# Kernel optimization log

Measured on AMD Instinct MI355X. Metric: run time of the kernel, lower is better.

Reference implementation:

```python
import jax, jax.numpy as jnp
import numpy as np

EPS = 1e-6

def _rms_norm(x, w):
    rms = jnp.sqrt(jnp.mean(x * x, axis=-1, keepdims=True) + EPS)
    return x / rms * w

def _rotate_half(x):
    x1, x2 = jnp.split(x, 2, axis=-1)
    return jnp.concatenate([-x2, x1], axis=-1)

def _apply_rope(qk, cos, sin):
    return qk * cos + _rotate_half(qk) * sin

def setup_inputs() -> dict:
    key = jax.random.key(0)
    ks = jax.random.split(key, 4)
    B, N, C, H = 4, 2048, 1024, 16
    hd = C // H
    x = jax.random.normal(ks[0], (B, N, C), dtype=jnp.float32)
    rope_cos = jax.random.uniform(ks[1], (1, 1, N, hd), dtype=jnp.float32)
    rope_sin = jax.random.uniform(ks[2], (1, 1, N, hd), dtype=jnp.float32)
    w_qkv = jax.random.normal(ks[3], (3 * C, C), dtype=jnp.float32) * (C ** -0.5)
    w_proj = jax.random.normal(jax.random.fold_in(key, 10), (C, C), dtype=jnp.float32) * (C ** -0.5)
    b_proj = jnp.zeros((C,), dtype=jnp.float32)
    q_norm_w = jnp.ones((hd,), dtype=jnp.float32)
    k_norm_w = jnp.ones((hd,), dtype=jnp.float32)
    return {"x": x, "rope_cos": rope_cos, "rope_sin": rope_sin, "w_qkv": w_qkv,
            "w_proj": w_proj, "b_proj": b_proj, "q_norm_w": q_norm_w, "k_norm_w": k_norm_w}

def reference(x, rope_cos, rope_sin, w_qkv, w_proj, b_proj, q_norm_w, k_norm_w):
    B, N, C = x.shape
    H = 16
    hd = C // H
    scale = hd ** -0.5
    qkv = jnp.einsum('bnc,dc->bnd', x, w_qkv)          # [B,N,3C]
    qkv = qkv.reshape(B, N, 3, H, hd).transpose(2, 0, 3, 1, 4)  # [3,B,H,N,hd]
    q, k, v = qkv[0], qkv[1], qkv[2]
    q = _rms_norm(q, q_norm_w)
    k = _rms_norm(k, k_norm_w)
    q = _apply_rope(q, rope_cos, rope_sin)
    k = _apply_rope(k, rope_cos, rope_sin)
    attn = jnp.einsum('bhqd,bhkd->bhqk', q, k) * scale
    attn = jax.nn.softmax(attn, axis=-1)
    out = jnp.einsum('bhqk,bhkd->bhqd', attn, v)        # [B,H,N,hd]
    out = out.transpose(0, 2, 1, 3).reshape(B, N, C)
    return jnp.einsum('bnc,dc->bnd', out, w_proj) + b_proj
```

## Files before the change

### kernel.cpp

```cpp
#include <hip/hip_runtime.h>
#include <stdint.h>
#include <math.h>

typedef unsigned short u16;
typedef __attribute__((ext_vector_type(8))) short short8;
typedef __attribute__((ext_vector_type(4))) float floatx4;
typedef __attribute__((ext_vector_type(4))) unsigned short ushort4v;

#define MFMA16(a, b, c) __builtin_amdgcn_mfma_f32_16x16x32_bf16(a, b, c, 0, 0, 0)

constexpr int B_ = 4, N_ = 2048, C_ = 1024, H_ = 16, HD = 64;
constexpr size_t SZ_X = (size_t)B_ * N_ * C_;
constexpr size_t SZ_WQKV = (size_t)3 * C_ * C_;
constexpr size_t SZ_WPROJ = (size_t)C_ * C_;
constexpr size_t SZ_QKV = (size_t)B_ * H_ * N_ * HD;

#define QSCALE 0.1803368801111204f

__device__ __forceinline__ u16 f2bf(float f) {
  union { float f; uint32_t u; } c; c.f = f;
  uint32_t u = c.u;
  return (u16)((u + 0x7FFFu + ((u >> 16) & 1u)) >> 16);
}
__device__ __forceinline__ uint32_t p2b(float s) {
  return (uint32_t)(int)__builtin_fmaf(s, 128.0f, 16250.91f);
}
__device__ __forceinline__ void async16(const u16* g, u16* l) {
  __builtin_amdgcn_global_load_lds(
      (const __attribute__((address_space(1))) void*)g,
      (__attribute__((address_space(3))) void*)l, 16, 0, 0);
}

__global__ __launch_bounds__(256) void cvt_all(
    const float* __restrict__ x, const float* __restrict__ wqkv,
    const float* __restrict__ wproj, u16* __restrict__ xb,
    u16* __restrict__ wqkvb, u16* __restrict__ wprojb) {
  const int n1 = (int)(SZ_X / 4), n2 = (int)(SZ_WQKV / 4);
  int i = blockIdx.x * 256 + threadIdx.x;
  const float* src;
  u16* dst;
  int k;
  if (i < n1) { src = x; dst = xb; k = i; }
  else if (i < n1 + n2) { src = wqkv; dst = wqkvb; k = i - n1; }
  else { src = wproj; dst = wprojb; k = i - n1 - n2; }
  float4 v = ((const float4*)src)[k];
  ushort4v o;
  o.x = f2bf(v.x); o.y = f2bf(v.y); o.z = f2bf(v.z); o.w = f2bf(v.w);
  ((ushort4v*)dst)[k] = o;
}

template <int MODE>
__global__ __launch_bounds__(256) void gemm_bt(
    const u16* __restrict__ A, const u16* __restrict__ Bm, int K,
    u16* __restrict__ qb, u16* __restrict__ kb, u16* __restrict__ vtb,
    float* __restrict__ outf, const float* __restrict__ bias, int N,
    const float* __restrict__ cosp, const float* __restrict__ sinp,
    const float* __restrict__ qw, const float* __restrict__ kw) {
  const int tid = threadIdx.x;
  const int wave = tid >> 6;
  const int lane = tid & 63;
  const int quad = lane >> 4;
  const int l16 = lane & 15;
  const int id = blockIdx.x + blockIdx.y * 64;
  const int bm0 = ((id & 7) * 8 + ((id >> 3) & 7)) * 128;
  const int bn0 = (id >> 6) * 128;
  const int wm = (wave >> 1) * 64;
  const int wn = (wave & 1) * 64;

  __shared__ __align__(16) u16 As[2][128 * 32];
  __shared__ __align__(16) u16 Bs[2][128 * 32];

  floatx4 acc[4][4];
#pragma unroll
  for (int i = 0; i < 4; ++i)
#pragma unroll
    for (int j = 0; j < 4; ++j)
#pragma unroll
      for (int r = 0; r < 4; ++r) acc[i][j][r] = 0.f;

  auto stage = [&](int k0, int buf) {
#pragma unroll
    for (int j = 0; j < 2; ++j) {
      const int seg = tid + j * 256;
      const int row = seg >> 2;
      const int ks = (seg & 3) * 8;
      u16* la = As[buf] + (size_t)(wave * 64 + j * 256) * 8;
      u16* lb = Bs[buf] + (size_t)(wave * 64 + j * 256) * 8;
      async16(A + (size_t)(bm0 + row) * K + k0 + ks, la);
      async16(Bm + (size_t)(bn0 + row) * K + k0 + ks, lb);
    }
  };

  const int niter = K >> 5;
  stage(0, 0);
  for (int kt = 0; kt < niter; ++kt) {
    __syncthreads();
    if (kt + 1 < niter) stage((kt + 1) << 5, (kt + 1) & 1);
    const u16* as = As[kt & 1];
    const u16* bs = Bs[kt & 1];

    short8 af[4], bf[4];
#pragma unroll
    for (int t = 0; t < 4; ++t)
      af[t] = *(const short8*)(as + (wm + t * 16 + l16) * 32 + quad * 8);
#pragma unroll
    for (int t = 0; t < 4; ++t)
      bf[t] = *(const short8*)(bs + (wn + t * 16 + l16) * 32 + quad * 8);
#pragma unroll
    for (int i = 0; i < 4; ++i)
#pragma unroll
      for (int j = 0; j < 4; ++j)
        acc[i][j] = MFMA16(af[i], bf[j], acc[i][j]);
  }

  if (MODE == 0) {
    const int hb = (bn0 + wn) >> 6;
    const int t = hb >> 4;
    const int h = hb & 15;
    if (t < 2) {
      const float* w = (t == 0) ? qw : kw;
      float wv[4];
#pragma unroll
      for (int j = 0; j < 4; ++j) wv[j] = w[j * 16 + l16];
#pragma unroll
      for (int i = 0; i < 4; ++i)
#pragma unroll
        for (int r = 0; r < 4; ++r) {
          const int m = bm0 + wm + i * 16 + quad * 4 + r;
          const int b = m >> 11, tok = m & 2047;
          float ss = 0.f;
#pragma unroll
          for (int j = 0; j < 4; ++j) ss += acc[i][j][r] * acc[i][j][r];
          ss += __shfl_xor(ss, 1);
          ss += __shfl_xor(ss, 2);
          ss += __shfl_xor(ss, 4);
          ss += __shfl_xor(ss, 8);
          const float inv = 1.0f / sqrtf(ss * (1.0f / 64.0f) + 1e-6f);
          float xn[4];
#pragma unroll
          for (int j = 0; j < 4; ++j) xn[j] = acc[i][j][r] * inv * wv[j];
          const size_t bh = (size_t)(b * 16 + h);
#pragma unroll
          for (int j = 0; j < 4; ++j) {
            const int e = j * 16 + l16;
            const float cs = cosp[tok * 64 + e];
            const float sn = sinp[tok * 64 + e];
            const float rot = (j < 2) ? -xn[j + 2] : xn[j - 2];
            float o = xn[j] * cs + rot * sn;
            if (t == 0) {
              qb[(bh * 2048 + tok) * 64 + e] = f2bf(o * QSCALE);
            } else {
              const int kt2 = tok >> 6, t3 = (tok >> 4) & 3;
              const int hf = j >> 1;
              const int qf = (j & 1) * 2 + (l16 >> 3);
              kb[bh * 131072 + (size_t)kt2 * 4096 + (t3 * 2 + hf) * 512 +
                 (qf * 16 + (tok & 15)) * 8 + (l16 & 7)] = f2bf(o);
            }
          }
        }
    } else {
#pragma unroll
      for (int i = 0; i < 4; ++i)
#pragma unroll
        for (int j = 0; j < 4; ++j)
#pragma unroll
          for (int r = 0; r < 4; ++r) {
            const int m = bm0 + wm + i * 16 + quad * 4 + r;
            const int b = m >> 11, tok = m & 2047;
            const int kt2 = tok >> 6, nn = tok & 63;
            const int hf = nn >> 5, qf = (nn & 31) >> 3, jf = nn & 7;
            vtb[(size_t)(b * 16 + h) * 131072 + (size_t)kt2 * 4096 +
                (j * 2 + hf) * 512 + (qf * 16 + l16) * 8 + jf] =
                f2bf(acc[i][j][r]);
          }
    }
  } else {
#pragma unroll
    for (int i = 0; i < 4; ++i)
#pragma unroll
      for (int j = 0; j < 4; ++j)
#pragma unroll
        for (int r = 0; r < 4; ++r) {
          const int m = bm0 + wm + i * 16 + quad * 4 + r;
          const int n = bn0 + wn + j * 16 + l16;
          outf[(size_t)m * N + n] = acc[i][j][r] + bias[n];
        }
  }
}

__global__ __launch_bounds__(256, 4) void attn_kernel(
    const u16* __restrict__ qb, const u16* __restrict__ kb,
    const u16* __restrict__ vtb, u16* __restrict__ ob) {
  const int tid = threadIdx.x;
  const int wave = tid >> 6, lane = tid & 63;
  const int quad = lane >> 4, l16 = lane & 15;

  const int id = blockIdx.x + blockIdx.y * 16;
  const int bh = (id & 7) + 8 * ((id >> 3) & 7);
  const int q0 = (id >> 6) * 128;

  __shared__ __align__(16) u16 Ksf[2][64 * 64];
  __shared__ __align__(16) u16 Ps[4][2][16 * 72];

  const u16* qptr = qb + (size_t)bh * (2048 * 64);
  const u16* kptr = kb + (size_t)bh * 131072;
  const u16* vptr = vtb + (size_t)bh * 131072;

  const int s0 = tid, s1 = tid + 256;
  const int lo0 = (wave * 64) * 8;
  const int lo1 = (256 + wave * 64) * 8;

  short8 aq[2][2];
#pragma unroll
  for (int sub = 0; sub < 2; ++sub) {
    const int qrow = q0 + wave * 32 + sub * 16 + l16;
#pragma unroll
    for (int hf = 0; hf < 2; ++hf)
      aq[sub][hf] =
          *(const short8*)(qptr + (size_t)qrow * 64 + hf * 32 + quad * 8);
  }

  short8 ones;
#pragma unroll
  for (int j = 0; j < 8; ++j) ones[j] = (short)0x3F80;

  floatx4 o[2][4], ol[2];
#pragma unroll
  for (int sub = 0; sub < 2; ++sub) {
#pragma unroll
    for (int r = 0; r < 4; ++r) ol[sub][r] = 0.f;
#pragma unroll
    for (int et = 0; et < 4; ++et)
#pragma unroll
      for (int r = 0; r < 4; ++r) o[sub][et][r] = 0.f;
  }

  async16(kptr + (size_t)s0 * 8, Ksf[0] + lo0);
  async16(kptr + (size_t)s1 * 8, Ksf[0] + lo1);

  for (int it = 0; it < 32; ++it) {
    __syncthreads();
    if (it + 1 < 32) {
      const u16* kt = kptr + (size_t)(it + 1) * 4096;
      const int b1 = (it + 1) & 1;
      async16(kt + (size_t)s0 * 8, Ksf[b1] + lo0);
      async16(kt + (size_t)s1 * 8, Ksf[b1] + lo1);
    }
    const u16* Kt = Ksf[it & 1];

    const u16* vt = vptr + (size_t)it * 4096;
    short8 vf[4][2];
#pragma unroll
    for (int et = 0; et < 4; ++et)
#pragma unroll
      for (int hf = 0; hf < 2; ++hf)
        vf[et][hf] =
            *(const short8*)(vt + (et * 2 + hf) * 512 + lane * 8);

#pragma unroll
    for (int t = 0; t < 4; ++t) {
      const short8 kf0 = *(const short8*)(Kt + t * 1024 + lane * 8);
      const short8 kf1 = *(const short8*)(Kt + t * 1024 + 512 + lane * 8);
#pragma unroll
      for (int sub = 0; sub < 2; ++sub) {
        floatx4 z;
#pragma unroll
        for (int r = 0; r < 4; ++r) z[r] = 0.f;
        z = MFMA16(kf0, aq[sub][0], z);
        z = MFMA16(kf1, aq[sub][1], z);
        uint2 w;
        w.x = p2b(z[0]) | (p2b(z[1]) << 16);
        w.y = p2b(z[2]) | (p2b(z[3]) << 16);
        *(uint2*)(Ps[wave][sub] + l16 * 72 + t * 16 + quad * 4) = w;
      }
    }

    __asm__ volatile("s_waitcnt lgkmcnt(0)" ::: "memory");

    short8 pa[2][2];
#pragma unroll
    for (int sub = 0; sub < 2; ++sub) {
      pa[sub][0] = *(const short8*)(Ps[wave][sub] + l16 * 72 + quad * 8);
      pa[sub][1] = *(const short8*)(Ps[wave][sub] + l16 * 72 + 32 + quad * 8);
    }

#pragma unroll
    for (int et = 0; et < 4; ++et)
#pragma unroll
      for (int sub = 0; sub < 2; ++sub) {
        o[sub][et] = MFMA16(pa[sub][0], vf[et][0], o[sub][et]);
        o[sub][et] = MFMA16(pa[sub][1], vf[et][1], o[sub][et]);
      }
#pragma unroll
    for (int sub = 0; sub < 2; ++sub) {
      ol[sub] = MFMA16(pa[sub][0], ones, ol[sub]);
      ol[sub] = MFMA16(pa[sub][1], ones, ol[sub]);
    }
  }

  const int b = bh >> 4, h = bh & 15;
#pragma unroll
  for (int sub = 0; sub < 2; ++sub) {
    float inv[4];
#pragma unroll
    for (int r = 0; r < 4; ++r) inv[r] = 1.0f / ol[sub][r];
#pragma unroll
    for (int et = 0; et < 4; ++et)
#pragma unroll
      for (int r = 0; r < 4; ++r) {
        const int row = q0 + wave * 32 + sub * 16 + quad * 4 + r;
        const int e = et * 16 + l16;
        ob[((size_t)b * 2048 + row) * 1024 + h * 64 + e] =
            f2bf(o[sub][et][r] * inv[r]);
      }
  }
}

extern "C" void kernel_launch(void* const* d_in, const int* in_sizes, int n_in,
                              void* d_out, int out_size, void* d_ws, size_t ws_size,
                              hipStream_t stream) {
  const float* x     = (const float*)d_in[0];
  const float* cosp  = (const float*)d_in[1];
  const float* sinp  = (const float*)d_in[2];
  const float* wqkv  = (const float*)d_in[3];
  const float* wproj = (const float*)d_in[4];
  const float* bias  = (const float*)d_in[5];
  const float* qw    = (const float*)d_in[6];
  const float* kw    = (const float*)d_in[7];
  float* out = (float*)d_out;

  u16* xb     = (u16*)d_ws;
  u16* wqkvb  = xb + SZ_X;
  u16* wprojb = wqkvb + SZ_WQKV;
  u16* qb     = wprojb + SZ_WPROJ;
  u16* kb     = qb + SZ_QKV;
  u16* vtb    = kb + SZ_QKV;
  u16* ob     = vtb + SZ_QKV;

  const int ncvt = (int)((SZ_X + SZ_WQKV + SZ_WPROJ) / 4 / 256);
  cvt_all<<<ncvt, 256, 0, stream>>>(x, wqkv, wproj, xb, wqkvb, wprojb);

  gemm_bt<0><<<dim3(64, 24), 256, 0, stream>>>(xb, wqkvb, 1024, qb, kb, vtb,
                                               nullptr, nullptr, 3072,
                                               cosp, sinp, qw, kw);
  attn_kernel<<<dim3(16, 64), 256, 0, stream>>>(qb, kb, vtb, ob);
  gemm_bt<1><<<dim3(64, 8), 256, 0, stream>>>(ob, wprojb, 1024, nullptr, nullptr,
                                              nullptr, out, bias, 1024,
                                              nullptr, nullptr, nullptr, nullptr);
}
```

Measured before the change: 296.8 us.

## Load K tiles directly from global in attention; interleave RoPE cos/sin

The attention kernel stops staging K tiles through double-buffered LDS with async global-to-LDS copies and instead reads K and V fragments straight from global memory (relying on cache) inside the loop, with a plain s_barrier in place of __syncthreads. V loads are moved next to their MFMAs to cut register pressure. Separately, the conversion kernel packs cos and sin into an interleaved float2 buffer so the QKV epilogue does one 8-byte load instead of two scalar loads. This trades LDS traffic and sync cost for possibly exposed global-load latency per iteration.

```diff
diff --git a/kernel.cpp b/kernel.cpp
--- a/kernel.cpp
+++ b/kernel.cpp
@@ -33,20 +33,35 @@
 
 __global__ __launch_bounds__(256) void cvt_all(
     const float* __restrict__ x, const float* __restrict__ wqkv,
-    const float* __restrict__ wproj, u16* __restrict__ xb,
-    u16* __restrict__ wqkvb, u16* __restrict__ wprojb) {
+    const float* __restrict__ wproj, const float* __restrict__ cosp,
+    const float* __restrict__ sinp, u16* __restrict__ xb,
+    u16* __restrict__ wqkvb, u16* __restrict__ wprojb,
+    float2* __restrict__ csb) {
   const int n1 = (int)(SZ_X / 4), n2 = (int)(SZ_WQKV / 4);
+  const int n3 = (int)(SZ_WPROJ / 4);
   int i = blockIdx.x * 256 + threadIdx.x;
-  const float* src;
-  u16* dst;
-  int k;
-  if (i < n1) { src = x; dst = xb; k = i; }
-  else if (i < n1 + n2) { src = wqkv; dst = wqkvb; k = i - n1; }
-  else { src = wproj; dst = wprojb; k = i - n1 - n2; }
-  float4 v = ((const float4*)src)[k];
-  ushort4v o;
-  o.x = f2bf(v.x); o.y = f2bf(v.y); o.z = f2bf(v.z); o.w = f2bf(v.w);
-  ((ushort4v*)dst)[k] = o;
+  if (i < n1 + n2 + n3) {
+    const float* src;
+    u16* dst;
+    int k;
+    if (i < n1) { src = x; dst = xb; k = i; }
+    else if (i < n1 + n2) { src = wqkv; dst = wqkvb; k = i - n1; }
+    else { src = wproj; dst = wprojb; k = i - n1 - n2; }
+    float4 v = ((const float4*)src)[k];
+    ushort4v o;
+    o.x = f2bf(v.x); o.y = f2bf(v.y); o.z = f2bf(v.z); o.w = f2bf(v.w);
+    ((ushort4v*)dst)[k] = o;
+  } else {
+    const int k = i - n1 - n2 - n3;
+    float4 c = ((const float4*)cosp)[k];
+    float4 s = ((const float4*)sinp)[k];
+    float4* d = (float4*)csb;
+    float4 o0, o1;
+    o0.x = c.x; o0.y = s.x; o0.z = c.y; o0.w = s.y;
+    o1.x = c.z; o1.y = s.z; o1.z = c.w; o1.w = s.w;
+    d[k * 2] = o0;
+    d[k * 2 + 1] = o1;
+  }
 }
 
 template <int MODE>
@@ -54,7 +69,7 @@
     const u16* __restrict__ A, const u16* __restrict__ Bm, int K,
     u16* __restrict__ qb, u16* __restrict__ kb, u16* __restrict__ vtb,
     float* __restrict__ outf, const float* __restrict__ bias, int N,
-    const float* __restrict__ cosp, const float* __restrict__ sinp,
+    const float2* __restrict__ csb,
     const float* __restrict__ qw, const float* __restrict__ kw) {
   const int tid = threadIdx.x;
   const int wave = tid >> 6;
@@ -143,10 +158,9 @@
 #pragma unroll
           for (int j = 0; j < 4; ++j) {
             const int e = j * 16 + l16;
-            const float cs = cosp[tok * 64 + e];
-            const float sn = sinp[tok * 64 + e];
+            const float2 cs = csb[tok * 64 + e];
             const float rot = (j < 2) ? -xn[j + 2] : xn[j - 2];
-            float o = xn[j] * cs + rot * sn;
+            float o = xn[j] * cs.x + rot * cs.y;
             if (t == 0) {
               qb[(bh * 2048 + tok) * 64 + e] = f2bf(o * QSCALE);
             } else {
@@ -199,17 +213,12 @@
   const int bh = (id & 7) + 8 * ((id >> 3) & 7);
   const int q0 = (id >> 6) * 128;
 
-  __shared__ __align__(16) u16 Ksf[2][64 * 64];
   __shared__ __align__(16) u16 Ps[4][2][16 * 72];
 
   const u16* qptr = qb + (size_t)bh * (2048 * 64);
   const u16* kptr = kb + (size_t)bh * 131072;
   const u16* vptr = vtb + (size_t)bh * 131072;
 
-  const int s0 = tid, s1 = tid + 256;
-  const int lo0 = (wave * 64) * 8;
-  const int lo1 = (256 + wave * 64) * 8;
-
   short8 aq[2][2];
 #pragma unroll
   for (int sub = 0; sub < 2; ++sub) {
@@ -235,32 +244,16 @@
       for (int r = 0; r < 4; ++r) o[sub][et][r] = 0.f;
   }
 
-  async16(kptr + (size_t)s0 * 8, Ksf[0] + lo0);
-  async16(kptr + (size_t)s1 * 8, Ksf[0] + lo1);
-
   for (int it = 0; it < 32; ++it) {
-    __syncthreads();
-    if (it + 1 < 32) {
-      const u16* kt = kptr + (size_t)(it + 1) * 4096;
-      const int b1 = (it + 1) & 1;
-      async16(kt + (size_t)s0 * 8, Ksf[b1] + lo0);
-      async16(kt + (size_t)s1 * 8, Ksf[b1] + lo1);
-    }
-    const u16* Kt = Ksf[it & 1];
-
+    __builtin_amdgcn_s_barrier();
+
+    const u16* kt = kptr + (size_t)it * 4096;
     const u16* vt = vptr + (size_t)it * 4096;
-    short8 vf[4][2];
-#pragma unroll
-    for (int et = 0; et < 4; ++et)
-#pragma unroll
-      for (int hf = 0; hf < 2; ++hf)
-        vf[et][hf] =
-            *(const short8*)(vt + (et * 2 + hf) * 512 + lane * 8);
 
 #pragma unroll
     for (int t = 0; t < 4; ++t) {
-      const short8 kf0 = *(const short8*)(Kt + t * 1024 + lane * 8);
-      const short8 kf1 = *(const short8*)(Kt + t * 1024 + 512 + lane * 8);
+      const short8 kf0 = *(const short8*)(kt + (t * 2) * 512 + lane * 8);
+      const short8 kf1 = *(const short8*)(kt + (t * 2 + 1) * 512 + lane * 8);
 #pragma unroll
       for (int sub = 0; sub < 2; ++sub) {
         floatx4 z;
@@ -285,12 +278,15 @@
     }
 
 #pragma unroll
-    for (int et = 0; et < 4; ++et)
+    for (int et = 0; et < 4; ++et) {
+      const short8 v0 = *(const short8*)(vt + (et * 2) * 512 + lane * 8);
+      const short8 v1 = *(const short8*)(vt + (et * 2 + 1) * 512 + lane * 8);
 #pragma unroll
       for (int sub = 0; sub < 2; ++sub) {
-        o[sub][et] = MFMA16(pa[sub][0], vf[et][0], o[sub][et]);
-        o[sub][et] = MFMA16(pa[sub][1], vf[et][1], o[sub][et]);
+        o[sub][et] = MFMA16(pa[sub][0], v0, o[sub][et]);
+        o[sub][et] = MFMA16(pa[sub][1], v1, o[sub][et]);
       }
+    }
 #pragma unroll
     for (int sub = 0; sub < 2; ++sub) {
       ol[sub] = MFMA16(pa[sub][0], ones, ol[sub]);
@@ -336,15 +332,18 @@
   u16* kb     = qb + SZ_QKV;
   u16* vtb    = kb + SZ_QKV;
   u16* ob     = vtb + SZ_QKV;
-
-  const int ncvt = (int)((SZ_X + SZ_WQKV + SZ_WPROJ) / 4 / 256);
-  cvt_all<<<ncvt, 256, 0, stream>>>(x, wqkv, wproj, xb, wqkvb, wprojb);
+  float2* csb = (float2*)(ob + SZ_X);
+
+  const int ncvt =
+      (int)((SZ_X + SZ_WQKV + SZ_WPROJ) / 4 + (size_t)(N_ * HD) / 4) / 256;
+  cvt_all<<<ncvt, 256, 0, stream>>>(x, wqkv, wproj, cosp, sinp,
+                                    xb, wqkvb, wprojb, csb);
 
   gemm_bt<0><<<dim3(64, 24), 256, 0, stream>>>(xb, wqkvb, 1024, qb, kb, vtb,
                                                nullptr, nullptr, 3072,
-                                               cosp, sinp, qw, kw);
+                                               csb, qw, kw);
   attn_kernel<<<dim3(16, 64), 256, 0, stream>>>(qb, kb, vtb, ob);
   gemm_bt<1><<<dim3(64, 8), 256, 0, stream>>>(ob, wprojb, 1024, nullptr, nullptr,
                                               nullptr, out, bias, 1024,
-                                              nullptr, nullptr, nullptr, nullptr);
-}
+                                              nullptr, nullptr, nullptr);
+}
```

New measurement: 301.8 us. Within noise of the previous version (+1.7%).
